# Kernel tuning notes

Hardware: AMD Instinct MI355X
Metric: run time of the kernel (lower is better)

Reference implementation:

```python
import jax, jax.numpy as jnp
import numpy as np

H = 256   # hidden_size
L = 6     # num_layers
IN = 128  # input_size
B = 128   # batch
T = 512   # seq_len


def setup_inputs() -> dict:
    key = jax.random.key(0)
    ks = jax.random.split(key, 9)
    s = 1.0 / np.sqrt(H)  # PyTorch LSTM init: U(-1/sqrt(H), 1/sqrt(H))
    x = jax.random.normal(ks[0], (B, T, IN), jnp.float32)
    h0 = jax.random.normal(ks[1], (L, B, H), jnp.float32)
    c0 = jax.random.normal(ks[2], (L, B, H), jnp.float32)
    w_ih0 = jax.random.uniform(ks[3], (4 * H, IN), jnp.float32, -s, s)
    w_ih = jax.random.uniform(ks[4], (L - 1, 4 * H, H), jnp.float32, -s, s)
    w_hh = jax.random.uniform(ks[5], (L, 4 * H, H), jnp.float32, -s, s)
    b_ih = jax.random.uniform(ks[6], (L, 4 * H), jnp.float32, -s, s)
    b_hh = jax.random.uniform(ks[7], (L, 4 * H), jnp.float32, -s, s)
    return {"x": x, "h0": h0, "c0": c0, "w_ih0": w_ih0, "w_ih": w_ih,
            "w_hh": w_hh, "b_ih": b_ih, "b_hh": b_hh}


def _lstm_layer(x, h0, c0, w_ih, w_hh, b):
    """One unidirectional LSTM layer. x: [B,T,Din] -> outputs [B,T,H], (hT, cT)."""
    # Precompute input contribution for all timesteps at once: [B,T,4H]
    xg = jnp.einsum('btd,gd->btg', x, w_ih) + b

    def step(carry, g_t):
        h, c = carry
        g = g_t + h @ w_hh.T  # [B,4H]
        i, f, gc, o = jnp.split(g, 4, axis=-1)  # PyTorch gate order i,f,g,o
        i = jax.nn.sigmoid(i)
        f = jax.nn.sigmoid(f)
        o = jax.nn.sigmoid(o)
        gc = jnp.tanh(gc)
        c = f * c + i * gc
        h = o * jnp.tanh(c)
        return (h, c), h

    (hT, cT), ys = jax.lax.scan(step, (h0, c0), jnp.swapaxes(xg, 0, 1))
    return jnp.swapaxes(ys, 0, 1), hT, cT


def reference(x, h0, c0, w_ih0, w_ih, w_hh, b_ih, b_hh):
    # Stacked 6-layer LSTM; fc / noop linear in the original is dead code.
    # Original returns state[0] (final hidden states, [L,B,H]) as float32.
    hs = []
    inp = x
    for l in range(L):
        wih_l = w_ih0 if l == 0 else w_ih[l - 1]
        b_l = b_ih[l] + b_hh[l]
        inp, hT, _ = _lstm_layer(inp, h0[l], c0[l], wih_l, w_hh[l], b_l)
        hs.append(hT)
    return jnp.stack(hs).astype(jnp.float32)  # [L, B, H]
```

## Files before the change

kernel.cpp:

```cpp
#include <hip/hip_runtime.h>

#define NLAYER 6
#define NB     128
#define NT     512
#define DIN    128
#define NH     256
#define NBLK   192
#define TSLOT_U64 (NB*NH/2)

typedef __attribute__((ext_vector_type(8))) short short8;
typedef __attribute__((ext_vector_type(4))) float f32x4;
typedef unsigned long long u64;

__device__ __forceinline__ unsigned f2bf2(float lo, float hi){
  unsigned a = __float_as_uint(lo), b = __float_as_uint(hi);
  a = (a + 0x7fffu + ((a>>16)&1u)) >> 16;
  b = (b + 0x7fffu + ((b>>16)&1u)) >> 16;
  return a | (b<<16);
}
__device__ __forceinline__ u64 f2bf4(float a, float b, float c, float d){
  return (u64)f2bf2(a,b) | ((u64)f2bf2(c,d) << 32);
}
__device__ __forceinline__ short8 pack16(u64 lo, u64 hi){
  union { u64 u[2]; short8 v; } w; w.u[0]=lo; w.u[1]=hi; return w.v;
}
__device__ __forceinline__ short8 ld8f_frag(const float* p){
  f32x4 a = *(const f32x4*)p;
  f32x4 b = *(const f32x4*)(p+4);
  return pack16(f2bf4(a[0],a[1],a[2],a[3]), f2bf4(b[0],b[1],b[2],b[3]));
}

__device__ __forceinline__ float sigmf(float v){ return 1.0f/(1.0f + __expf(-v)); }
__device__ __forceinline__ float tanhfast(float v){
  v = fminf(fmaxf(v, -15.0f), 15.0f);
  float e = __expf(2.0f*v);
  return (e - 1.0f)/(e + 1.0f);
}

__device__ __forceinline__ int ld_flag(const int* p){
  return __hip_atomic_load(p, __ATOMIC_RELAXED, __HIP_MEMORY_SCOPE_AGENT);
}
__device__ __forceinline__ void st_flag(int* p, int v){
  __hip_atomic_store(p, v, __ATOMIC_RELAXED, __HIP_MEMORY_SCOPE_AGENT);
}
__device__ __forceinline__ u64 ring_ld(const u64* p){
  return __hip_atomic_load(p, __ATOMIC_RELAXED, __HIP_MEMORY_SCOPE_AGENT);
}
__device__ __forceinline__ void ring_st(u64* p, u64 v){
  __hip_atomic_store(p, v, __ATOMIC_RELAXED, __HIP_MEMORY_SCOPE_AGENT);
}

__device__ __forceinline__ unsigned tagw(float f, unsigned tag){
  unsigned a = __float_as_uint(f);
  return ((a + 0x7fffu + ((a>>16)&1u)) & 0xffff0000u) | tag;
}
__device__ __forceinline__ unsigned strip2(u64 q){
  return __builtin_amdgcn_perm((unsigned)(q>>32), (unsigned)q, 0x07060302u);
}

__device__ __forceinline__ short8 lds_frag(const unsigned* __restrict__ buf, int row, int soff){
  return *(const short8*)((const short*)buf + row*264 + soff);
}

template<int NKX>
__device__ __forceinline__ void lstm_run(
    const float* __restrict__ x,  const float* __restrict__ h0,
    const float* __restrict__ c0, const float* __restrict__ wx,
    const float* __restrict__ wh, const float* __restrict__ bi,
    const float* __restrict__ bh, float* __restrict__ out,
    int* __restrict__ acks, u64* __restrict__ ring, unsigned (*ldsb)[2112],
    int Wv, int l, int bg, int s, int wv, int lane)
{
  constexpr int KIT  = NKX + 8;
  constexpr int KX   = NKX*32;
  constexpr bool HASX = (NKX == 8);
  const int l15  = lane & 15;
  const int quad = lane >> 4;
  const int bloc = bg*16 + l15;
  const int jcol = s*16 + quad*4;
  const int Wm   = Wv - 1;

  short8 A[4][KIT];
  #pragma unroll
  for (int q = 0; q < 4; ++q){
    const float* wrow_x = wx + (size_t)(q*NH + s*16 + l15)*KX;
    const float* wrow_h = wh + (size_t)(q*NH + s*16 + l15)*NH;
    #pragma unroll
    for (int kt = 0; kt < KIT; ++kt){
      int k0 = kt*32 + quad*8;
      A[q][kt] = (k0 < KX) ? ld8f_frag(wrow_x + k0)
                           : ld8f_frag(wrow_h + (k0 - KX));
    }
  }

  f32x4 bsv[4];
  #pragma unroll
  for (int q = 0; q < 4; ++q){
    f32x4 a = *(const f32x4*)(bi + q*NH + jcol);
    f32x4 b = *(const f32x4*)(bh + q*NH + jcol);
    bsv[q] = a + b;
  }
  float cc[4];
  {
    f32x4 cv = *(const f32x4*)(c0 + ((size_t)l*NB + bloc)*NH + jcol);
    cc[0]=cv[0]; cc[1]=cv[1]; cc[2]=cv[2]; cc[3]=cv[3];
  }

  const int* ackOwn = acks + (l*8 + bg)*16;
  int* ackPrevW = HASX ? acks + ((l-1)*8 + bg)*16 + s : nullptr;
  const u64* ringPrev = HASX ? ring + (size_t)(l-1)*Wv*TSLOT_U64 : nullptr;
  u64*       ringOwn  = ring + (size_t)l*Wv*TSLOT_U64;
  const bool lastL = (l == NLAYER-1);
  const bool wrap  = (Wv < NT);
  int ackmin = 0;

  const int sbase = wv*512 + lane*2;

  for (int t = 0; t < NT; ++t){
    const int slot  = t & Wm;
    const int pslot = (t-1) & Wm;

    if (wrap && !lastL && t >= Wv){
      const int need = t - Wv + 1;
      if (ackmin < need){
        int v = 0, guard = 0;
        for (;;){
          v = (lane < 16) ? ld_flag(ackOwn + lane) : 0x7fffffff;
          if (__ballot(v >= need) == ~0ull) break;
          __builtin_amdgcn_s_sleep(1);
          if (++guard > (1<<22)) break;
        }
        int m = v;
        #pragma unroll
        for (int o = 8; o; o >>= 1) m = min(m, __shfl_xor(m, o));
        ackmin = __shfl(m, 0);
      }
    }

    short8 Bx[NKX];
    if constexpr (!HASX){
      const float* px = x + ((size_t)bloc*NT + t)*DIN + quad*8;
      #pragma unroll
      for (int k = 0; k < NKX; ++k) Bx[k] = ld8f_frag(px + k*32);
    }

    const u64* srcX = HASX ? ringPrev + (size_t)slot*TSLOT_U64 + bg*2048 : nullptr;
    const u64* srcH = (t > 0) ? ringOwn + (size_t)pslot*TSLOT_U64 + bg*2048 : nullptr;
    unsigned* ldsX = ldsb[(t&1)*2 + 0];
    unsigned* ldsH = ldsb[(t&1)*2 + 1];
    u64 qx[8], qh[8];
    {
      bool okx = !HASX, okh = (srcH == nullptr);
      const u64 tx2 = (u64)(unsigned)(t+1) * 0x0000000100000001ull;
      const u64 th2 = (u64)(unsigned)t     * 0x0000000100000001ull;
      int guard = 0;
      while (!(okx & okh)){
        if (!okh){
          #pragma unroll
          for (int c = 0; c < 4; ++c){
            qh[c*2]   = ring_ld(srcH + sbase + c*128);
            qh[c*2+1] = ring_ld(srcH + sbase + c*128 + 1);
          }
        }
        if (!okx){
          #pragma unroll
          for (int c = 0; c < 4; ++c){
            qx[c*2]   = ring_ld(srcX + sbase + c*128);
            qx[c*2+1] = ring_ld(srcX + sbase + c*128 + 1);
          }
        }
        if (!okh){
          u64 m = 0;
          #pragma unroll
          for (int i = 0; i < 8; ++i) m |= qh[i] ^ th2;
          okh = (__ballot(((unsigned)(m | (m>>32)) & 0xffffu) == 0u) == ~0ull);
        }
        if (!okx){
          u64 m = 0;
          #pragma unroll
          for (int i = 0; i < 8; ++i) m |= qx[i] ^ tx2;
          okx = (__ballot(((unsigned)(m | (m>>32)) & 0xffffu) == 0u) == ~0ull);
        }
        if (okx & okh) break;
        if ((++guard & 7) == 7) __builtin_amdgcn_s_sleep(1);
        if (guard > (1<<22)) break;
      }
    }
    if constexpr (HASX){
      #pragma unroll
      for (int c = 0; c < 4; ++c)
        *(u64*)(ldsX + (wv*4+c)*132 + lane*2) =
            (u64)strip2(qx[c*2]) | ((u64)strip2(qx[c*2+1]) << 32);
    }
    if (srcH){
      #pragma unroll
      for (int c = 0; c < 4; ++c)
        *(u64*)(ldsH + (wv*4+c)*132 + lane*2) =
            (u64)strip2(qh[c*2]) | ((u64)strip2(qh[c*2+1]) << 32);
    }
    __syncthreads();

    if (HASX && wrap && ((t & 7) == 7) && lane == 0) st_flag(ackPrevW, t+1);

    if constexpr (HASX){
      #pragma unroll
      for (int k = 0; k < NKX; ++k) Bx[k] = lds_frag(ldsX, l15, quad*8 + k*32);
    }
    short8 Bh[8];
    if (t == 0){
      const float* ph = h0 + ((size_t)l*NB + bloc)*NH + quad*8;
      #pragma unroll
      for (int k = 0; k < 8; ++k) Bh[k] = ld8f_frag(ph + k*32);
    } else {
      #pragma unroll
      for (int k = 0; k < 8; ++k) Bh[k] = lds_frag(ldsH, l15, quad*8 + k*32);
    }

    f32x4 a0 = {0,0,0,0}, a1 = {0,0,0,0}, a2 = {0,0,0,0}, a3 = {0,0,0,0};
    #pragma unroll
    for (int k = 0; k < NKX; ++k){
      a0 = __builtin_amdgcn_mfma_f32_16x16x32_bf16(A[0][k], Bx[k], a0, 0, 0, 0);
      a1 = __builtin_amdgcn_mfma_f32_16x16x32_bf16(A[1][k], Bx[k], a1, 0, 0, 0);
      a2 = __builtin_amdgcn_mfma_f32_16x16x32_bf16(A[2][k], Bx[k], a2, 0, 0, 0);
      a3 = __builtin_amdgcn_mfma_f32_16x16x32_bf16(A[3][k], Bx[k], a3, 0, 0, 0);
    }
    #pragma unroll
    for (int k = 0; k < 8; ++k){
      a0 = __builtin_amdgcn_mfma_f32_16x16x32_bf16(A[0][NKX+k], Bh[k], a0, 0, 0, 0);
      a1 = __builtin_amdgcn_mfma_f32_16x16x32_bf16(A[1][NKX+k], Bh[k], a1, 0, 0, 0);
      a2 = __builtin_amdgcn_mfma_f32_16x16x32_bf16(A[2][NKX+k], Bh[k], a2, 0, 0, 0);
      a3 = __builtin_amdgcn_mfma_f32_16x16x32_bf16(A[3][NKX+k], Bh[k], a3, 0, 0, 0);
    }

    u64* hp = ringOwn + (size_t)slot*TSLOT_U64 + (size_t)bloc*128 + s*8 + quad*2;
    const unsigned otag = (unsigned)(t+1);
    float hv[4];
    #pragma unroll
    for (int r = 0; r < 2; ++r){
      float ig = sigmf(a0[r] + bsv[0][r]);
      float fg = sigmf(a1[r] + bsv[1][r]);
      float gv = tanhfast(a2[r] + bsv[2][r]);
      float og = sigmf(a3[r] + bsv[3][r]);
      float cn = fg*cc[r] + ig*gv;
      cc[r] = cn;
      hv[r] = og * tanhfast(cn);
    }
    ring_st(hp, (u64)tagw(hv[0], otag) | ((u64)tagw(hv[1], otag) << 32));
    #pragma unroll
    for (int r = 2; r < 4; ++r){
      float ig = sigmf(a0[r] + bsv[0][r]);
      float fg = sigmf(a1[r] + bsv[1][r]);
      float gv = tanhfast(a2[r] + bsv[2][r]);
      float og = sigmf(a3[r] + bsv[3][r]);
      float cn = fg*cc[r] + ig*gv;
      cc[r] = cn;
      hv[r] = og * tanhfast(cn);
    }
    ring_st(hp + 1, (u64)tagw(hv[2], otag) | ((u64)tagw(hv[3], otag) << 32));

    if (t == NT-1){
      f32x4 ov; ov[0]=hv[0]; ov[1]=hv[1]; ov[2]=hv[2]; ov[3]=hv[3];
      *(f32x4*)(out + ((size_t)l*NB + bloc)*NH + jcol) = ov;
    }
  }
}

__global__ __launch_bounds__(256, 1)
void lstm_pipe(const float* __restrict__ x,   const float* __restrict__ h0,
               const float* __restrict__ c0,  const float* __restrict__ wih0,
               const float* __restrict__ wih, const float* __restrict__ whh,
               const float* __restrict__ bih, const float* __restrict__ bhh,
               float* __restrict__ out, int* __restrict__ acks,
               u64* __restrict__ ring, int Wv)
{
  __shared__ unsigned ldsb[4][2112];
  const int bid  = blockIdx.x;
  const int bg   = bid & 7;
  const int j    = bid >> 3;
  const int l    = j >> 2;
  const int b    = j & 3;
  const int lane = threadIdx.x & 63;
  const int wv   = threadIdx.x >> 6;
  const int s    = b*4 + wv;

  if (l == 0)
    lstm_run<4>(x, h0, c0, wih0, whh, bih, bhh,
                out, acks, ring, ldsb, Wv, 0, bg, s, wv, lane);
  else
    lstm_run<8>(x, h0, c0,
                wih + (size_t)(l-1)*(4*NH*NH),
                whh + (size_t)l*(4*NH*NH),
                bih + (size_t)l*(4*NH),
                bhh + (size_t)l*(4*NH),
                out, acks, ring, ldsb, Wv, l, bg, s, wv, lane);
}

extern "C" void kernel_launch(void* const* d_in, const int* in_sizes, int n_in,
                              void* d_out, int out_size, void* d_ws, size_t ws_size,
                              hipStream_t stream)
{
  (void)in_sizes; (void)n_in; (void)out_size;
  const float* x    = (const float*)d_in[0];
  const float* h0   = (const float*)d_in[1];
  const float* c0   = (const float*)d_in[2];
  const float* wih0 = (const float*)d_in[3];
  const float* wih  = (const float*)d_in[4];
  const float* whh  = (const float*)d_in[5];
  const float* bih  = (const float*)d_in[6];
  const float* bhh  = (const float*)d_in[7];

  int Wv = 32;
  size_t ringB;
  for (;;){
    ringB = (size_t)NLAYER*Wv*TSLOT_U64*8;
    if (8192 + ringB <= ws_size || Wv <= 8) break;
    Wv >>= 1;
  }

  int* acks = (int*)d_ws;
  u64* ring = (u64*)((char*)d_ws + 8192);

  (void)hipMemsetAsync(d_ws, 0, 8192 + ringB, stream);
  hipLaunchKernelGGL(lstm_pipe, dim3(NBLK), dim3(256), 0, stream,
                     x, h0, c0, wih0, wih, whh, bih, bhh,
                     (float*)d_out, acks, ring, Wv);
}
```

Baseline: 1.923 ms.

## Prefetch next-step input ring slot and write own hidden slice directly to LDS

Issues the ring loads for the next timestep's input (from the previous layer) before the MFMA work, and if the tags already match, stages them into the next LDS buffer so the next iteration can skip polling for X. Each block also writes its own bf16 hidden-state slice straight into the next LDS H buffer, and the lanes that own that slice skip the ring poll and load. The aim is to take global-memory polling latency off the recurrent critical path. The cost is extra registers for the prefetched values, and it relies on a subtle LDS ownership and synchronisation layout that could race between the own-slice write and other waves reading the buffer.

```diff
diff --git a/kernel.cpp b/kernel.cpp
--- a/kernel.cpp
+++ b/kernel.cpp
@@ -78,6 +78,8 @@
   const int quad = lane >> 4;
   const int bloc = bg*16 + l15;
   const int jcol = s*16 + quad*4;
+  const int b    = s >> 2;
+  const bool ownl = ((lane >> 4) == b);
   const int Wm   = Wv - 1;
 
   short8 A[4][KIT];
@@ -97,8 +99,8 @@
   #pragma unroll
   for (int q = 0; q < 4; ++q){
     f32x4 a = *(const f32x4*)(bi + q*NH + jcol);
-    f32x4 b = *(const f32x4*)(bh + q*NH + jcol);
-    bsv[q] = a + b;
+    f32x4 b2 = *(const f32x4*)(bh + q*NH + jcol);
+    bsv[q] = a + b2;
   }
   float cc[4];
   {
@@ -113,6 +115,7 @@
   const bool lastL = (l == NLAYER-1);
   const bool wrap  = (Wv < NT);
   int ackmin = 0;
+  bool pfx = false;
 
   const int sbase = wv*512 + lane*2;
 
@@ -148,14 +151,19 @@
     const u64* srcH = (t > 0) ? ringOwn + (size_t)pslot*TSLOT_U64 + bg*2048 : nullptr;
     unsigned* ldsX = ldsb[(t&1)*2 + 0];
     unsigned* ldsH = ldsb[(t&1)*2 + 1];
+    const bool xFromLoop = HASX && !pfx;
     u64 qx[8], qh[8];
     {
-      bool okx = !HASX, okh = (srcH == nullptr);
+      bool okx = !xFromLoop, okh = (srcH == nullptr);
       const u64 tx2 = (u64)(unsigned)(t+1) * 0x0000000100000001ull;
       const u64 th2 = (u64)(unsigned)t     * 0x0000000100000001ull;
+      if (ownl){
+        #pragma unroll
+        for (int i = 0; i < 8; ++i) qh[i] = th2;
+      }
       int guard = 0;
       while (!(okx & okh)){
-        if (!okh){
+        if (!okh && !ownl){
           #pragma unroll
           for (int c = 0; c < 4; ++c){
             qh[c*2]   = ring_ld(srcH + sbase + c*128);
@@ -186,13 +194,13 @@
         if (guard > (1<<22)) break;
       }
     }
-    if constexpr (HASX){
+    if (xFromLoop){
       #pragma unroll
       for (int c = 0; c < 4; ++c)
         *(u64*)(ldsX + (wv*4+c)*132 + lane*2) =
             (u64)strip2(qx[c*2]) | ((u64)strip2(qx[c*2+1]) << 32);
     }
-    if (srcH){
+    if (srcH && !ownl){
       #pragma unroll
       for (int c = 0; c < 4; ++c)
         *(u64*)(ldsH + (wv*4+c)*132 + lane*2) =
@@ -214,6 +222,17 @@
     } else {
       #pragma unroll
       for (int k = 0; k < 8; ++k) Bh[k] = lds_frag(ldsH, l15, quad*8 + k*32);
+    }
+
+    u64 qpx[8];
+    const bool dopf = HASX && (t+1 < NT);
+    if (dopf){
+      const u64* srcXn = ringPrev + (size_t)((t+1)&Wm)*TSLOT_U64 + bg*2048;
+      #pragma unroll
+      for (int c = 0; c < 4; ++c){
+        qpx[c*2]   = ring_ld(srcXn + sbase + c*128);
+        qpx[c*2+1] = ring_ld(srcXn + sbase + c*128 + 1);
+      }
     }
 
     f32x4 a0 = {0,0,0,0}, a1 = {0,0,0,0}, a2 = {0,0,0,0}, a3 = {0,0,0,0};
@@ -258,9 +277,30 @@
     }
     ring_st(hp + 1, (u64)tagw(hv[2], otag) | ((u64)tagw(hv[3], otag) << 32));
 
+    *(u64*)(ldsb[((t+1)&1)*2 + 1] + l15*132 + s*8 + quad*2) =
+        f2bf4(hv[0], hv[1], hv[2], hv[3]);
+
     if (t == NT-1){
       f32x4 ov; ov[0]=hv[0]; ov[1]=hv[1]; ov[2]=hv[2]; ov[3]=hv[3];
       *(f32x4*)(out + ((size_t)l*NB + bloc)*NH + jcol) = ov;
+    }
+
+    if (dopf){
+      const u64 txn = (u64)(unsigned)(t+2) * 0x0000000100000001ull;
+      u64 m = 0;
+      #pragma unroll
+      for (int i = 0; i < 8; ++i) m |= qpx[i] ^ txn;
+      const bool hit = (__ballot(((unsigned)(m | (m>>32)) & 0xffffu) == 0u) == ~0ull);
+      if (hit){
+        unsigned* ldsXn = ldsb[((t+1)&1)*2 + 0];
+        #pragma unroll
+        for (int c = 0; c < 4; ++c)
+          *(u64*)(ldsXn + (wv*4+c)*132 + lane*2) =
+              (u64)strip2(qpx[c*2]) | ((u64)strip2(qpx[c*2+1]) << 32);
+      }
+      pfx = hit;
+    } else {
+      pfx = false;
     }
   }
 }
```

Measured after the change: 2.779 ms. 44.5% more time.
